# Kernel optimization log

Measured on AMD Instinct MI355X. Metric: run time of the kernel, lower is better.

Reference implementation:

```python
import jax, jax.numpy as jnp
import numpy as np
import math

N_STATIONS = 50  # N in [N, 7, 56] causal matrix


def setup_inputs() -> dict:
    key = jax.random.key(0)
    k1, k2, k3, k4 = jax.random.split(key, 4)
    B, L, H, E = 3200, 7, 8, 64
    S, D = 56, 64
    queries = jax.random.normal(k1, (B, L, H, E), dtype=jnp.float32)
    keys = jax.random.normal(k2, (B, S, H, E), dtype=jnp.float32)
    values = jax.random.normal(k3, (B, S, H, D), dtype=jnp.float32)
    # station-specific multiplicative causal matrix in [0, 1]
    attn_mask = jax.random.uniform(k4, (N_STATIONS, L, S), dtype=jnp.float32)
    return {"queries": queries, "keys": keys, "values": values, "attn_mask": attn_mask}


def reference(queries, keys, values, attn_mask):
    B, L, H, E = queries.shape
    S = values.shape[1]
    N = attn_mask.shape[0]  # number of stations; B % N == 0
    ab = B // N  # actual batch size per station group
    scale = 1.0 / math.sqrt(E)
    # raw scores [B, H, L, S]
    scores = jnp.einsum('blhe,bshe->bhls', queries, keys)
    # multiplicative station-specific mask: reshape batch into (ab, N) and
    # broadcast mask [N, L, S] over (ab, H)
    masked = scores.reshape(ab, N, H, L, S) * attn_mask[None, :, None, :, :]
    masked = masked.reshape(B, H, L, S)
    # note: scale is applied AFTER masking, as in the original module
    A = jax.nn.softmax(scale * masked, axis=-1)  # dropout is identity at eval
    V = jnp.einsum('bhls,bshd->blhd', A, values)
    return V
```

## Files before the change

kernel.cpp:

```cpp
#include <hip/hip_runtime.h>
#include <math.h>


typedef __attribute__((ext_vector_type(8))) _Float16 half8;

#define GLDS(gp, lp) __builtin_amdgcn_global_load_lds(                        \
    (const __attribute__((address_space(1))) void*)(gp),                      \
    (__attribute__((address_space(3))) void*)(lp), 16, 0, 0)

__launch_bounds__(128, 4)
__global__ void fullattn_kernel(const float* __restrict__ q,
                                const float* __restrict__ k,
                                const float* __restrict__ v,
                                const float* __restrict__ mask,
                                float* __restrict__ out,
                                int nstations) {
    __shared__ __align__(16) float    KL2[2][56 * 64];
    __shared__ __align__(16) float    VL2[2][56 * 64];
    __shared__ __align__(16) _Float16 QL2[2][7 * 64];

    const int lane = threadIdx.x & 63;
    const int wid  = __builtin_amdgcn_readfirstlane(threadIdx.x >> 6);
    float*    KL = KL2[wid];
    float*    VL = VL2[wid];
    _Float16* QL = QL2[wid];

    const int unit = blockIdx.x * 2 + wid;
    const int b    = unit >> 3;
    const int h    = unit & 7;
    const int st   = b % nstations;

    const int kbase = b * 28672 + h * 64;
    const int qbase = b * 3584  + h * 64;

    const int rr = lane >> 4;
    const int pp = lane & 15;

#pragma unroll
    for (int j = 0; j < 14; ++j) {
        const int row = j * 4 + rr;
        const int c   = pp ^ (row & 15);
        GLDS(k + kbase + row * 512 + c * 4, (char*)KL + j * 1024);
    }
    __builtin_amdgcn_sched_barrier(0);

    float qr[7];
#pragma unroll
    for (int l = 0; l < 7; ++l) qr[l] = q[qbase + l * 512 + lane];
    __builtin_amdgcn_sched_barrier(0);

    const int ml = (lane < 56) ? lane : 55;
    float m[7];
#pragma unroll
    for (int l = 0; l < 7; ++l)
        m[l] = mask[st * 392 + l * 56 + ml] * 0.125f;
    __builtin_amdgcn_sched_barrier(0);

#pragma unroll
    for (int j = 0; j < 14; ++j) {
        const int row = j * 4 + rr;
        GLDS(v + kbase + row * 512 + pp * 4, (char*)VL + j * 1024);
    }
    __builtin_amdgcn_sched_barrier(0);

    asm volatile("s_waitcnt vmcnt(28)" ::: "memory");
    __builtin_amdgcn_sched_barrier(0);

#pragma unroll
    for (int l = 0; l < 7; ++l) QL[l * 64 + lane] = (_Float16)qr[l];

    const int x16 = ml & 15;
    float acc[7];
#pragma unroll
    for (int l = 0; l < 7; ++l) acc[l] = 0.0f;

#pragma unroll
    for (int c2 = 0; c2 < 8; ++c2) {
        const float4 kv0 = *(const float4*)(&KL[ml * 64 + (((2 * c2)     ^ x16) << 2)]);
        const float4 kv1 = *(const float4*)(&KL[ml * 64 + (((2 * c2 + 1) ^ x16) << 2)]);
#pragma unroll
        for (int l = 0; l < 7; ++l) {
            const half8 qv = *(const half8*)(&QL[l * 64 + c2 * 8]);
            acc[l] = fmaf(kv0.x, (float)qv[0], acc[l]);
            acc[l] = fmaf(kv0.y, (float)qv[1], acc[l]);
            acc[l] = fmaf(kv0.z, (float)qv[2], acc[l]);
            acc[l] = fmaf(kv0.w, (float)qv[3], acc[l]);
            acc[l] = fmaf(kv1.x, (float)qv[4], acc[l]);
            acc[l] = fmaf(kv1.y, (float)qv[5], acc[l]);
            acc[l] = fmaf(kv1.z, (float)qv[6], acc[l]);
            acc[l] = fmaf(kv1.w, (float)qv[7], acc[l]);
        }
    }

    float* pbuf = KL;
    float rdenom[7];
#pragma unroll
    for (int l = 0; l < 7; ++l) {
        const float sc = acc[l] * m[l];
        const float p  = (lane < 56) ? __expf(sc) : 0.0f;
        float sum = p;
#pragma unroll
        for (int off = 32; off >= 1; off >>= 1)
            sum += __shfl_xor(sum, off);
        pbuf[l * 64 + lane] = p;
        rdenom[l] = __builtin_amdgcn_rcpf(sum);
    }

    asm volatile("s_waitcnt vmcnt(0)" ::: "memory");
    __builtin_amdgcn_sched_barrier(0);

    float facc[7];
#pragma unroll
    for (int l = 0; l < 7; ++l) facc[l] = 0.0f;

#pragma unroll
    for (int s4 = 0; s4 < 14; ++s4) {
        const float vv0 = VL[(s4 * 4 + 0) * 64 + lane];
        const float vv1 = VL[(s4 * 4 + 1) * 64 + lane];
        const float vv2 = VL[(s4 * 4 + 2) * 64 + lane];
        const float vv3 = VL[(s4 * 4 + 3) * 64 + lane];
#pragma unroll
        for (int l = 0; l < 7; ++l) {
            const float4 p4 = *(const float4*)(&pbuf[l * 64 + s4 * 4]);
            facc[l] = fmaf(p4.x, vv0, facc[l]);
            facc[l] = fmaf(p4.y, vv1, facc[l]);
            facc[l] = fmaf(p4.z, vv2, facc[l]);
            facc[l] = fmaf(p4.w, vv3, facc[l]);
        }
    }

#pragma unroll
    for (int l = 0; l < 7; ++l)
        out[qbase + l * 512 + lane] = facc[l] * rdenom[l];
}

extern "C" void kernel_launch(void* const* d_in, const int* in_sizes, int n_in,
                              void* d_out, int out_size, void* d_ws, size_t ws_size,
                              hipStream_t stream) {
    const float* q    = (const float*)d_in[0];
    const float* k    = (const float*)d_in[1];
    const float* v    = (const float*)d_in[2];
    const float* mask = (const float*)d_in[3];
    float* out        = (float*)d_out;

    const int B = in_sizes[0] / (7 * 8 * 64);
    const int nstations = in_sizes[3] / (7 * 56);
    const int nunits = B * 8;

    fullattn_kernel<<<dim3(nunits / 2), dim3(128), 0, stream>>>(q, k, v, mask, out, nstations);
}
```

Baseline: 169.7 us.

## Stream V through registers in rotating chunks and launch one wave per block

V is no longer staged in LDS through async global-to-LDS copies. It is loaded straight into three rotating 8-row register buffers that are refilled while the P·V accumulation proceeds. Blocks shrink to a single 64-thread wave, and LDS per block drops to only K and Q. This is meant to cut LDS footprint and raise occupancy, overlapping V loads with compute. In exchange it uses more VGPRs and relies on the hand-set vmcnt(22) staying correct for the new load ordering.

```diff
diff --git a/kernel.cpp b/kernel.cpp
--- a/kernel.cpp
+++ b/kernel.cpp
@@ -8,24 +8,18 @@
     (const __attribute__((address_space(1))) void*)(gp),                      \
     (__attribute__((address_space(3))) void*)(lp), 16, 0, 0)
 
-__launch_bounds__(128, 4)
+__launch_bounds__(64, 2)
 __global__ void fullattn_kernel(const float* __restrict__ q,
                                 const float* __restrict__ k,
                                 const float* __restrict__ v,
                                 const float* __restrict__ mask,
                                 float* __restrict__ out,
                                 int nstations) {
-    __shared__ __align__(16) float    KL2[2][56 * 64];
-    __shared__ __align__(16) float    VL2[2][56 * 64];
-    __shared__ __align__(16) _Float16 QL2[2][7 * 64];
+    __shared__ __align__(16) float    KL[56 * 64];
+    __shared__ __align__(16) _Float16 QL[7 * 64];
 
-    const int lane = threadIdx.x & 63;
-    const int wid  = __builtin_amdgcn_readfirstlane(threadIdx.x >> 6);
-    float*    KL = KL2[wid];
-    float*    VL = VL2[wid];
-    _Float16* QL = QL2[wid];
-
-    const int unit = blockIdx.x * 2 + wid;
+    const int lane = threadIdx.x;
+    const int unit = blockIdx.x;
     const int b    = unit >> 3;
     const int h    = unit & 7;
     const int st   = b % nstations;
@@ -56,14 +50,12 @@
         m[l] = mask[st * 392 + l * 56 + ml] * 0.125f;
     __builtin_amdgcn_sched_barrier(0);
 
+    float vA[8], vB[8], vC[8];
 #pragma unroll
-    for (int j = 0; j < 14; ++j) {
-        const int row = j * 4 + rr;
-        GLDS(v + kbase + row * 512 + pp * 4, (char*)VL + j * 1024);
-    }
+    for (int i = 0; i < 8; ++i) vA[i] = v[kbase + i * 512 + lane];
     __builtin_amdgcn_sched_barrier(0);
 
-    asm volatile("s_waitcnt vmcnt(28)" ::: "memory");
+    asm volatile("s_waitcnt vmcnt(22)" ::: "memory");
     __builtin_amdgcn_sched_barrier(0);
 
 #pragma unroll
@@ -92,6 +84,11 @@
         }
     }
 
+#pragma unroll
+    for (int i = 0; i < 8; ++i) vB[i] = v[kbase + (8 + i) * 512 + lane];
+#pragma unroll
+    for (int i = 0; i < 8; ++i) vC[i] = v[kbase + (16 + i) * 512 + lane];
+
     float* pbuf = KL;
     float rdenom[7];
 #pragma unroll
@@ -106,28 +103,37 @@
         rdenom[l] = __builtin_amdgcn_rcpf(sum);
     }
 
-    asm volatile("s_waitcnt vmcnt(0)" ::: "memory");
-    __builtin_amdgcn_sched_barrier(0);
-
     float facc[7];
 #pragma unroll
     for (int l = 0; l < 7; ++l) facc[l] = 0.0f;
 
-#pragma unroll
-    for (int s4 = 0; s4 < 14; ++s4) {
-        const float vv0 = VL[(s4 * 4 + 0) * 64 + lane];
-        const float vv1 = VL[(s4 * 4 + 1) * 64 + lane];
-        const float vv2 = VL[(s4 * 4 + 2) * 64 + lane];
-        const float vv3 = VL[(s4 * 4 + 3) * 64 + lane];
+    auto pvg = [&](const float (&vw)[8], int g) {
 #pragma unroll
         for (int l = 0; l < 7; ++l) {
-            const float4 p4 = *(const float4*)(&pbuf[l * 64 + s4 * 4]);
-            facc[l] = fmaf(p4.x, vv0, facc[l]);
-            facc[l] = fmaf(p4.y, vv1, facc[l]);
-            facc[l] = fmaf(p4.z, vv2, facc[l]);
-            facc[l] = fmaf(p4.w, vv3, facc[l]);
+            const float4 p0 = *(const float4*)(&pbuf[l * 64 + g * 8]);
+            const float4 p1 = *(const float4*)(&pbuf[l * 64 + g * 8 + 4]);
+            facc[l] = fmaf(p0.x, vw[0], facc[l]);
+            facc[l] = fmaf(p0.y, vw[1], facc[l]);
+            facc[l] = fmaf(p0.z, vw[2], facc[l]);
+            facc[l] = fmaf(p0.w, vw[3], facc[l]);
+            facc[l] = fmaf(p1.x, vw[4], facc[l]);
+            facc[l] = fmaf(p1.y, vw[5], facc[l]);
+            facc[l] = fmaf(p1.z, vw[6], facc[l]);
+            facc[l] = fmaf(p1.w, vw[7], facc[l]);
         }
-    }
+    };
+    auto ldv = [&](float (&vw)[8], int row0) {
+#pragma unroll
+        for (int i = 0; i < 8; ++i) vw[i] = v[kbase + (row0 + i) * 512 + lane];
+    };
+
+    pvg(vA, 0); ldv(vA, 24);
+    pvg(vB, 1); ldv(vB, 32);
+    pvg(vC, 2); ldv(vC, 40);
+    pvg(vA, 3); ldv(vA, 48);
+    pvg(vB, 4);
+    pvg(vC, 5);
+    pvg(vA, 6);
 
 #pragma unroll
     for (int l = 0; l < 7; ++l)
@@ -145,7 +151,6 @@
 
     const int B = in_sizes[0] / (7 * 8 * 64);
     const int nstations = in_sizes[3] / (7 * 56);
-    const int nunits = B * 8;
 
-    fullattn_kernel<<<dim3(nunits / 2), dim3(128), 0, stream>>>(q, k, v, mask, out, nstations);
+    fullattn_kernel<<<dim3(B * 8), dim3(64), 0, stream>>>(q, k, v, mask, out, nstations);
 }
```

After: 166.2 us. 1.02x faster.
